# Kernel tuning notes

Measured on AMD Instinct MI355X. Metric: run time of the kernel, lower is better.

## Reference

```python
import jax, jax.numpy as jnp
import numpy as np

N_NODES = 100000
N_EDGES = 1600000
N_GRAPHS = 128


def setup_inputs() -> dict:
    key = jax.random.key(0)
    ks = jax.random.split(key, 8)
    x = jax.random.normal(ks[0], (N_NODES, 384), dtype=jnp.float32)
    edge_index = jax.random.randint(ks[1], (2, N_EDGES), 0, N_NODES, dtype=jnp.int64)
    batch = jnp.sort(jax.random.randint(ks[2], (N_NODES,), 0, N_GRAPHS, dtype=jnp.int64))
    W1 = jax.random.normal(ks[3], (384, 128), dtype=jnp.float32) * (1.0 / np.sqrt(384))
    b1 = jnp.zeros((128,), dtype=jnp.float32)
    W2 = jax.random.normal(ks[4], (128, 64), dtype=jnp.float32) * (1.0 / np.sqrt(128))
    b2 = jnp.zeros((64,), dtype=jnp.float32)
    Wlin = jax.random.normal(ks[5], (64, 2), dtype=jnp.float32) * (1.0 / np.sqrt(64))
    blin = jnp.zeros((2,), dtype=jnp.float32)
    return {"x": x, "edge_index": edge_index, "batch": batch,
            "W1": W1, "b1": b1, "W2": W2, "b2": b2, "Wlin": Wlin, "blin": blin}


def gcn_conv(x, src, dst, W, b, n_nodes):
    # PyG GCNConv: self-loops + symmetric normalization D^{-1/2} A_hat D^{-1/2},
    # linear transform first (out_dim < in_dim -> cheaper messages).
    h = x @ W  # [N, out]
    deg = jax.ops.segment_sum(jnp.ones_like(dst, dtype=h.dtype), dst,
                              num_segments=n_nodes) + 1.0  # self-loop weight
    dis = jax.lax.rsqrt(deg)  # deg >= 1 always (self-loop)
    norm = dis[src] * dis[dst]  # per-edge normalization [E]
    msg = h[src] * norm[:, None]  # gather + scale [E, out]
    agg = jax.ops.segment_sum(msg, dst, num_segments=n_nodes)
    agg = agg + h * (dis * dis)[:, None]  # self-loop contribution
    return agg + b


def reference(x, edge_index, batch, W1, b1, W2, b2, Wlin, blin):
    src, dst = edge_index[0], edge_index[1]
    n_nodes = x.shape[0]
    h = jax.nn.relu(gcn_conv(x, src, dst, W1, b1, n_nodes))
    h = jax.nn.relu(gcn_conv(h, src, dst, W2, b2, n_nodes))
    # global_mean_pool over graph ids
    sums = jax.ops.segment_sum(h, batch, num_segments=N_GRAPHS)
    cnts = jax.ops.segment_sum(jnp.ones((n_nodes,), dtype=h.dtype), batch,
                               num_segments=N_GRAPHS)
    pooled = sums / jnp.maximum(cnts, 1.0)[:, None]  # [G, 64]
    # dropout is identity in eval mode
    return pooled @ Wlin + blin  # [G, 2]
```

## Files before the change

### kernel.cpp

```cpp
#include <hip/hip_runtime.h>


#define NN 100000
#define NG 128
#define BNODES 256
#define NBUK ((NN + BNODES - 1) / BNODES)
#define BCAP 6144

typedef __attribute__((ext_vector_type(8))) short short8;
typedef __attribute__((ext_vector_type(8))) unsigned short u16x8;
typedef __attribute__((ext_vector_type(4))) float f32x4;

__device__ __forceinline__ unsigned short f2bf(float f) {
    union { float f; unsigned u; } v; v.f = f;
    unsigned r = v.u + 0x7fffu + ((v.u >> 16) & 1u);
    return (unsigned short)(r >> 16);
}
__device__ __forceinline__ float bf2f(unsigned short h) {
    union { unsigned u; float f; } v; v.u = ((unsigned)h) << 16;
    return v.f;
}

__device__ __forceinline__ void gload_lds16(const float* g, void* l) {
    __builtin_amdgcn_global_load_lds(
        (const __attribute__((address_space(1))) void*)g,
        (__attribute__((address_space(3))) void*)l, 16, 0, 0);
}

__global__ __launch_bounds__(256) void init_kernel(int* __restrict__ bcnt,
                                                   float* __restrict__ pooled,
                                                   float* __restrict__ cnt) {
    const int i = blockIdx.x * 256 + threadIdx.x;
    if (i < NBUK) bcnt[i] = 0;
    if (i < NG * 64) pooled[i] = 0.f;
    if (i < NG) cnt[i] = 0.f;
}

__global__ __launch_bounds__(256) void bucket_scatter(const int* __restrict__ src,
                                                      const int* __restrict__ dst,
                                                      int* __restrict__ bcnt,
                                                      int2* __restrict__ pairs, int E) {
    __shared__ int hist[NBUK];
    __shared__ int lbase[NBUK];
    __shared__ int lfill[NBUK];
    const int t = threadIdx.x;
    const int chunk = (E + gridDim.x - 1) / gridDim.x;
    const int lo = blockIdx.x * chunk;
    const int hi = min(E, lo + chunk);
    for (int b = t; b < NBUK; b += 256) { hist[b] = 0; lfill[b] = 0; }
    __syncthreads();
    for (int i = lo + t; i < hi; i += 256)
        atomicAdd(&hist[dst[i] >> 8], 1);
    __syncthreads();
    for (int b = t; b < NBUK; b += 256)
        lbase[b] = hist[b] ? atomicAdd(&bcnt[b], hist[b]) : 0;
    __syncthreads();
    for (int i = lo + t; i < hi; i += 256) {
        const int s = src[i], d = dst[i];
        const int b = d >> 8;
        const int off = atomicAdd(&lfill[b], 1);
        pairs[(size_t)b * BCAP + lbase[b] + off] = make_int2(s, d);
    }
}

__global__ __launch_bounds__(512) void bucket_scan(const int* __restrict__ bcnt,
                                                   int* __restrict__ bbase,
                                                   int* __restrict__ rowptr,
                                                   int N, int E) {
    __shared__ int sm[512];
    const int t = threadIdx.x;
    sm[t] = (t < NBUK) ? bcnt[t] : 0;
    __syncthreads();
    for (int d = 1; d < 512; d <<= 1) {
        int a = (t >= d) ? sm[t - d] : 0;
        __syncthreads();
        sm[t] += a;
        __syncthreads();
    }
    if (t <= NBUK) bbase[t] = (t == 0) ? 0 : sm[t - 1];
    if (t == 0) rowptr[N] = E;
}

__global__ __launch_bounds__(256) void bucket_build(const int2* __restrict__ pairs,
                                                    const int* __restrict__ bcnt,
                                                    const int* __restrict__ bbase,
                                                    int* __restrict__ rowptr,
                                                    float* __restrict__ dis,
                                                    int* __restrict__ col, int N) {
    __shared__ int cnt[BNODES];
    __shared__ int sm[BNODES];
    __shared__ int pref[BNODES];
    __shared__ int fillc[BNODES];
    const int b = blockIdx.x;
    const int t = threadIdx.x;
    const int nbase = b * BNODES;
    const int ecnt = bcnt[b];
    const int2* ep = pairs + (size_t)b * BCAP;
    const int gbase = bbase[b];

    cnt[t] = 0;
    fillc[t] = 0;
    __syncthreads();
    for (int i = t; i < ecnt; i += 256)
        atomicAdd(&cnt[ep[i].y & (BNODES - 1)], 1);
    __syncthreads();
    sm[t] = cnt[t];
    __syncthreads();
    for (int d = 1; d < 256; d <<= 1) {
        int a = (t >= d) ? sm[t - d] : 0;
        __syncthreads();
        sm[t] += a;
        __syncthreads();
    }
    pref[t] = sm[t] - cnt[t];
    const int node = nbase + t;
    if (node < N) {
        rowptr[node] = gbase + pref[t];
        dis[node] = rsqrtf((float)cnt[t] + 1.0f);
    }
    __syncthreads();
    for (int i = t; i < ecnt; i += 256) {
        const int2 e = ep[i];
        const int d = e.y & (BNODES - 1);
        const int pos = gbase + pref[d] + atomicAdd(&fillc[d], 1);
        col[pos] = e.x;
    }
}

__global__ __launch_bounds__(256) void pack_w(const float* __restrict__ W,
                                              unsigned short* __restrict__ packH,
                                              unsigned short* __restrict__ packL,
                                              int K, int BN) {
    const int idx = blockIdx.x * blockDim.x + threadIdx.x;
    if (idx >= K * BN) return;
    const int e = idx & 7;
    const int l = (idx >> 3) & 63;
    const int rest = idx >> 9;
    const int NF = BN >> 4;
    const int nf = rest % NF;
    const int ks = rest / NF;
    const int n = nf * 16 + (l & 15);
    const int k = ks * 32 + ((l >> 4) & 3) * 8 + e;
    const float v = W[(size_t)k * BN + n];
    const unsigned short h = f2bf(v);
    packH[idx] = h;
    packL[idx] = f2bf(v - bf2f(h));
}

template <int BN, int K>
__global__ __launch_bounds__(256) void gemm_mfma(const float* __restrict__ A,
                                                 const unsigned short* __restrict__ WpH,
                                                 const unsigned short* __restrict__ WpL,
                                                 const float* __restrict__ scale,
                                                 unsigned short* __restrict__ Out,
                                                 int N) {
    constexpr int BM = 64;
    constexpr int NK = K / 32;
    constexpr int WROWS = (BN == 128) ? 2 : 4;
    constexpr int WCOLS = (BN == 128) ? 2 : 1;
    constexpr int WTM = BM / WROWS;
    constexpr int MF = WTM / 16;
    constexpr int NFW = (BN / WCOLS) / 16;
    constexpr int NFB = BN / 16;

    __shared__ float AsF[4][4][16][32];

    const int t = threadIdx.x;
    const int wid = t >> 6, lane = t & 63;
    const int wr = wid / WCOLS, wc = wid % WCOLS;
    const int r0 = blockIdx.x * BM;

    const int dmarow0 = min(r0 + wid * 16 + (lane >> 3), NN - 1);
    const int dmarow1 = min(r0 + wid * 16 + 8 + (lane >> 3), NN - 1);
    const float* dmap0 = A + (size_t)dmarow0 * K + (lane & 7) * 4;
    const float* dmap1 = A + (size_t)dmarow1 * K + (lane & 7) * 4;

    auto stageA = [&](int buf, int ks) {
        gload_lds16(dmap0 + ks * 32, &AsF[buf][wid][0][0]);
        gload_lds16(dmap1 + ks * 32, &AsF[buf][wid][8][0]);
    };
    auto loadB = [&](int ks, short8* bH, short8* bL) {
#pragma unroll
        for (int n = 0; n < NFW; ++n) {
            const int nfg = wc * NFW + n;
            const int base = ((ks * NFB + nfg) * 64 + lane) * 8;
            bH[n] = *(const short8*)&WpH[base];
            bL[n] = *(const short8*)&WpL[base];
        }
    };

    f32x4 acc[MF][NFW];
#pragma unroll
    for (int m = 0; m < MF; ++m)
#pragma unroll
        for (int n = 0; n < NFW; ++n) acc[m][n] = (f32x4){0.f, 0.f, 0.f, 0.f};

    short8 bHc[NFW], bLc[NFW];
    loadB(0, bHc, bLc);
    stageA(0, 0);
    if (NK > 1) stageA(1, 1);
    if (NK > 2) stageA(2, 2);

#pragma unroll
    for (int ks = 0; ks < NK; ++ks) {
        if (ks == NK - 1) {
            asm volatile("s_waitcnt vmcnt(0)" ::: "memory");
        } else {
            asm volatile("s_waitcnt vmcnt(4)" ::: "memory");
        }
        __builtin_amdgcn_s_barrier();
        short8 bHn[NFW], bLn[NFW];
        if (ks + 1 < NK) loadB(ks + 1, bHn, bLn);
        if (ks + 3 < NK) stageA((ks + 3) & 3, ks + 3);
        const int cur = ks & 3;
#pragma unroll
        for (int m = 0; m < MF; ++m) {
            const int mf = wr * MF + m;
            const float* fp = &AsF[cur][mf][lane & 15][(lane >> 4) * 8];
            const f32x4 f0 = *(const f32x4*)fp;
            const f32x4 f1 = *(const f32x4*)(fp + 4);
            short8 aH;
            aH[0] = (short)f2bf(f0[0]);
            aH[1] = (short)f2bf(f0[1]);
            aH[2] = (short)f2bf(f0[2]);
            aH[3] = (short)f2bf(f0[3]);
            aH[4] = (short)f2bf(f1[0]);
            aH[5] = (short)f2bf(f1[1]);
            aH[6] = (short)f2bf(f1[2]);
            aH[7] = (short)f2bf(f1[3]);
#pragma unroll
            for (int n = 0; n < NFW; ++n) {
                acc[m][n] = __builtin_amdgcn_mfma_f32_16x16x32_bf16(aH, bHc[n], acc[m][n], 0, 0, 0);
                acc[m][n] = __builtin_amdgcn_mfma_f32_16x16x32_bf16(aH, bLc[n], acc[m][n], 0, 0, 0);
            }
        }
        if (ks + 1 < NK) {
#pragma unroll
            for (int n = 0; n < NFW; ++n) {
                bHc[n] = bHn[n];
                bLc[n] = bLn[n];
            }
        }
    }

#pragma unroll
    for (int m = 0; m < MF; ++m) {
        const int row0 = r0 + wr * WTM + m * 16 + ((lane >> 4) << 2);
        float sc[4];
#pragma unroll
        for (int r = 0; r < 4; ++r) sc[r] = (row0 + r < N) ? scale[row0 + r] : 0.f;
#pragma unroll
        for (int n = 0; n < NFW; ++n) {
            const int cn = wc * (NFW * 16) + n * 16 + (lane & 15);
#pragma unroll
            for (int r = 0; r < 4; ++r) {
                if (row0 + r < N)
                    Out[(size_t)(row0 + r) * BN + cn] = f2bf(acc[m][n][r] * sc[r]);
            }
        }
    }
}

template <int COLS>
__global__ __launch_bounds__(256) void agg_gather(const int* __restrict__ rowptr,
                                                  const int* __restrict__ col,
                                                  const float* __restrict__ dis,
                                                  const unsigned short* __restrict__ Hs,
                                                  const float* __restrict__ bias,
                                                  float* __restrict__ Out, int N) {
    constexpr int NPW = (COLS == 128) ? 1 : 2;
    constexpr int LPN = 64 / NPW;
    constexpr int LPR = COLS / 8;
    constexpr int NSG = LPN / LPR;
    const int gw = (int)((blockIdx.x * blockDim.x + threadIdx.x) >> 6);
    const int lane = threadIdx.x & 63;
    const int sub = lane / LPN;
    const int nl = lane % LPN;
    const int esub = nl / LPR;
    const int sl = nl % LPR;
    const int node = gw * NPW + sub;
    const int lgbase = sub * LPN;

    float acc[8];
#pragma unroll
    for (int k = 0; k < 8; ++k) acc[k] = 0.f;

    int base = 0, len = 0;
    const int nodec = (node < N) ? node : 0;
    if (node < N) {
        base = rowptr[node];
        len = rowptr[node + 1] - base;
    }

    for (int j0 = 0; j0 < len; j0 += LPN) {
        const int remain = min(LPN, len - j0);
        const int sidx = (nl < remain) ? col[base + j0 + nl] : nodec;
        const int qtr = (remain + NSG - 1) / NSG;
        const int off = esub * qtr;
        int u = 0;
        for (; u + 8 <= qtr; u += 8) {
            u16x8 hv[8];
            float wv[8];
#pragma unroll
            for (int b = 0; b < 8; ++b) {
                const int idx = off + u + b;
                const int s = __shfl(sidx, lgbase + idx);
                wv[b] = (idx < remain) ? 1.f : 0.f;
                hv[b] = *(const u16x8*)(Hs + (size_t)s * COLS + sl * 8);
            }
#pragma unroll
            for (int b = 0; b < 8; ++b)
#pragma unroll
                for (int k = 0; k < 8; ++k)
                    acc[k] = fmaf(bf2f(hv[b][k]), wv[b], acc[k]);
        }
        for (; u + 4 <= qtr; u += 4) {
            u16x8 hv[4];
            float wv[4];
#pragma unroll
            for (int b = 0; b < 4; ++b) {
                const int idx = off + u + b;
                const int s = __shfl(sidx, lgbase + idx);
                wv[b] = (idx < remain) ? 1.f : 0.f;
                hv[b] = *(const u16x8*)(Hs + (size_t)s * COLS + sl * 8);
            }
#pragma unroll
            for (int b = 0; b < 4; ++b)
#pragma unroll
                for (int k = 0; k < 8; ++k)
                    acc[k] = fmaf(bf2f(hv[b][k]), wv[b], acc[k]);
        }
        for (; u < qtr; ++u) {
            const int idx = off + u;
            const int s = __shfl(sidx, lgbase + idx);
            const float w = (idx < remain) ? 1.f : 0.f;
            const u16x8 hv = *(const u16x8*)(Hs + (size_t)s * COLS + sl * 8);
#pragma unroll
            for (int k = 0; k < 8; ++k)
                acc[k] = fmaf(bf2f(hv[k]), w, acc[k]);
        }
    }

#pragma unroll
    for (int k = 0; k < 8; ++k) {
        acc[k] += __shfl_xor(acc[k], LPR);
        acc[k] += __shfl_xor(acc[k], 2 * LPR);
    }

    if (node < N && esub == 0) {
        const float dd = dis[node];
        const u16x8 hsb = *(const u16x8*)(Hs + (size_t)node * COLS + sl * 8);
        const f32x4 bv0 = *(const f32x4*)(bias + sl * 8);
        const f32x4 bv1 = *(const f32x4*)(bias + sl * 8 + 4);
        f32x4 o0, o1;
#pragma unroll
        for (int k = 0; k < 4; ++k) {
            o0[k] = fmaxf(fmaf(acc[k] + bf2f(hsb[k]), dd, bv0[k]), 0.f);
            o1[k] = fmaxf(fmaf(acc[k + 4] + bf2f(hsb[k + 4]), dd, bv1[k]), 0.f);
        }
        *(f32x4*)(Out + (size_t)node * COLS + sl * 8) = o0;
        *(f32x4*)(Out + (size_t)node * COLS + sl * 8 + 4) = o1;
    }
}

__global__ __launch_bounds__(256) void pool_kernel(const float* __restrict__ H,
                                                   const int* __restrict__ batch,
                                                   float* __restrict__ pooled,
                                                   float* __restrict__ cnt, int N) {
    const int c = threadIdx.x & 63;
    const int w = threadIdx.x >> 6;
    const int row0 = blockIdx.x * 128 + w * 32;
    if (row0 >= N) return;
    const int nr = min(32, N - row0);

    float v[32];
    int b[32];
#pragma unroll
    for (int i = 0; i < 32; ++i) {
        const int r = row0 + i;
        if (i < nr) {
            v[i] = H[(size_t)r * 64 + c];
            b[i] = batch[r];
        } else {
            v[i] = 0.f;
            b[i] = -1;
        }
    }
    int cur = b[0];
    float sum = 0.f, csum = 0.f;
#pragma unroll
    for (int i = 0; i < 32; ++i) {
        if (i < nr) {
            if (b[i] != cur) {
                atomicAdd(&pooled[cur * 64 + c], sum);
                if (c == 0) atomicAdd(&cnt[cur], csum);
                cur = b[i];
                sum = 0.f;
                csum = 0.f;
            }
            sum += v[i];
            csum += 1.f;
        }
    }
    atomicAdd(&pooled[cur * 64 + c], sum);
    if (c == 0) atomicAdd(&cnt[cur], csum);
}

__global__ __launch_bounds__(256) void final_kernel(const float* __restrict__ pooled,
                                                    const float* __restrict__ cnt,
                                                    const float* __restrict__ Wlin,
                                                    const float* __restrict__ blin,
                                                    float* __restrict__ out) {
    const int t = threadIdx.x;
    const int g = t >> 1, o = t & 1;
    const float inv = 1.0f / fmaxf(cnt[g], 1.0f);
    float s = 0.f;
#pragma unroll
    for (int j = 0; j < 64; ++j) s = fmaf(pooled[g * 64 + j], Wlin[j * 2 + o], s);
    out[t] = s * inv + blin[o];
}

extern "C" void kernel_launch(void* const* d_in, const int* in_sizes, int n_in,
                              void* d_out, int out_size, void* d_ws, size_t ws_size,
                              hipStream_t stream) {
    const float* x     = (const float*)d_in[0];
    const int*   edge  = (const int*)d_in[1];
    const int*   batch = (const int*)d_in[2];
    const float* W1    = (const float*)d_in[3];
    const float* b1    = (const float*)d_in[4];
    const float* W2    = (const float*)d_in[5];
    const float* b2    = (const float*)d_in[6];
    const float* Wlin  = (const float*)d_in[7];
    const float* blin  = (const float*)d_in[8];
    float* out = (float*)d_out;

    const int N = NN;
    const int E = in_sizes[1] / 2;
    const int* src = edge;
    const int* dst = edge + E;

    char* ws = (char*)d_ws;
    size_t off = 0;
    auto alloc = [&](size_t bytes) -> void* {
        void* p = ws + off;
        off += (bytes + 511) & ~(size_t)511;
        return p;
    };
    float* dis    = (float*)alloc((size_t)N * 4);
    int*   rowptr = (int*)alloc((size_t)(N + 1) * 4);
    int*   bcnt   = (int*)alloc((size_t)NBUK * 4);
    int*   bbase  = (int*)alloc((size_t)(NBUK + 1) * 4);
    int*   col    = (int*)alloc((size_t)E * 4);
    int2*  pairs  = (int2*)alloc((size_t)NBUK * BCAP * 8);
    unsigned short* w1h = (unsigned short*)alloc((size_t)384 * 128 * 2);
    unsigned short* w1l = (unsigned short*)alloc((size_t)384 * 128 * 2);
    unsigned short* w2h = (unsigned short*)alloc((size_t)128 * 64 * 2);
    unsigned short* w2l = (unsigned short*)alloc((size_t)128 * 64 * 2);
    unsigned short* h1bf = (unsigned short*)alloc((size_t)N * 128 * 2);
    float* agg1   = (float*)alloc((size_t)N * 128 * 4);
    float* pooled = (float*)alloc((size_t)NG * 64 * 4);
    float* cnt    = (float*)alloc((size_t)NG * 4);
    unsigned short* h2bf = h1bf;
    float* agg2 = agg1;

    init_kernel<<<(NG * 64 + 255) / 256, 256, 0, stream>>>(bcnt, pooled, cnt);

    pack_w<<<(384 * 128 + 255) / 256, 256, 0, stream>>>(W1, w1h, w1l, 384, 128);
    pack_w<<<(128 * 64 + 255) / 256, 256, 0, stream>>>(W2, w2h, w2l, 128, 64);

    bucket_scatter<<<512, 256, 0, stream>>>(src, dst, bcnt, pairs, E);
    bucket_scan<<<1, 512, 0, stream>>>(bcnt, bbase, rowptr, N, E);
    bucket_build<<<NBUK, 256, 0, stream>>>(pairs, bcnt, bbase, rowptr, dis, col, N);

    const int gblocks = (N + 63) / 64;
    gemm_mfma<128, 384><<<gblocks, 256, 0, stream>>>(x, w1h, w1l, dis, h1bf, N);
    agg_gather<128><<<(N + 3) / 4, 256, 0, stream>>>(rowptr, col, dis, h1bf, b1, agg1, N);

    gemm_mfma<64, 128><<<gblocks, 256, 0, stream>>>(agg1, w2h, w2l, dis, h2bf, N);
    agg_gather<64><<<(N + 7) / 8, 256, 0, stream>>>(rowptr, col, dis, h2bf, b2, agg2, N);

    pool_kernel<<<(N + 127) / 128, 256, 0, stream>>>(agg2, batch, pooled, cnt, N);
    final_kernel<<<1, 256, 0, stream>>>(pooled, cnt, Wlin, blin, out);
}
```

Baseline: 243.3 us.

## Store layer-1 aggregation output in bf16 and add bf16-input GEMM for layer 2

The first aggregation kernel now writes its ReLU output as bf16 instead of fp32, halving that intermediate's write and the second GEMM's read traffic. A new GEMM variant consumes the bf16 activations directly via global-to-LDS loads with a 4-stage buffer, skipping the hi/lo split of A and using only the two MFMAs against the hi and lo weight halves. The cost is extra rounding error on the layer-1 activations, and agg2 now aliases the bf16 buffer, which is sized for 128 bf16 columns and so fits exactly the 64 fp32 columns it holds.

```diff
diff --git a/kernel.cpp b/kernel.cpp
--- a/kernel.cpp
+++ b/kernel.cpp
@@ -21,7 +21,7 @@
     return v.f;
 }
 
-__device__ __forceinline__ void gload_lds16(const float* g, void* l) {
+__device__ __forceinline__ void gload_lds16(const void* g, void* l) {
     __builtin_amdgcn_global_load_lds(
         (const __attribute__((address_space(1))) void*)g,
         (__attribute__((address_space(3))) void*)l, 16, 0, 0);
@@ -261,13 +261,103 @@
     }
 }
 
-template <int COLS>
+template <int BN, int K>
+__global__ __launch_bounds__(256) void gemm_mfma_b(const unsigned short* __restrict__ A,
+                                                   const unsigned short* __restrict__ WpH,
+                                                   const unsigned short* __restrict__ WpL,
+                                                   const float* __restrict__ scale,
+                                                   unsigned short* __restrict__ Out,
+                                                   int N) {
+    constexpr int BM = 64;
+    constexpr int NK = K / 32;
+    constexpr int WROWS = 4;
+    constexpr int WTM = BM / WROWS;
+    constexpr int NFW = BN / 16;
+    constexpr int NFB = BN / 16;
+
+    __shared__ unsigned short AsB[4][4][16][32];
+
+    const int t = threadIdx.x;
+    const int wid = t >> 6, lane = t & 63;
+    const int wr = wid;
+    const int r0 = blockIdx.x * BM;
+
+    const int dmarow = min(r0 + wid * 16 + (lane >> 2), NN - 1);
+    const unsigned short* dmap = A + (size_t)dmarow * K + (lane & 3) * 8;
+
+    auto stageA = [&](int buf, int ks) {
+        gload_lds16(dmap + ks * 32, &AsB[buf][wid][0][0]);
+    };
+    auto loadB = [&](int ks, short8* bH, short8* bL) {
+#pragma unroll
+        for (int n = 0; n < NFW; ++n) {
+            const int base = ((ks * NFB + n) * 64 + lane) * 8;
+            bH[n] = *(const short8*)&WpH[base];
+            bL[n] = *(const short8*)&WpL[base];
+        }
+    };
+
+    f32x4 acc[NFW];
+#pragma unroll
+    for (int n = 0; n < NFW; ++n) acc[n] = (f32x4){0.f, 0.f, 0.f, 0.f};
+
+    short8 bHc[NFW], bLc[NFW];
+    loadB(0, bHc, bLc);
+    stageA(0, 0);
+    if (NK > 1) stageA(1, 1);
+    if (NK > 2) stageA(2, 2);
+
+#pragma unroll
+    for (int ks = 0; ks < NK; ++ks) {
+        if (ks == NK - 1) {
+            asm volatile("s_waitcnt vmcnt(0)" ::: "memory");
+        } else if (ks == 0) {
+            asm volatile("s_waitcnt vmcnt(2)" ::: "memory");
+        } else {
+            asm volatile("s_waitcnt vmcnt(4)" ::: "memory");
+        }
+        __builtin_amdgcn_s_barrier();
+        short8 bHn[NFW], bLn[NFW];
+        if (ks + 1 < NK) loadB(ks + 1, bHn, bLn);
+        if (ks + 3 < NK) stageA((ks + 3) & 3, ks + 3);
+        const int cur = ks & 3;
+        const short8 aH = *(const short8*)&AsB[cur][wr][lane & 15][(lane >> 4) * 8];
+#pragma unroll
+        for (int n = 0; n < NFW; ++n) {
+            acc[n] = __builtin_amdgcn_mfma_f32_16x16x32_bf16(aH, bHc[n], acc[n], 0, 0, 0);
+            acc[n] = __builtin_amdgcn_mfma_f32_16x16x32_bf16(aH, bLc[n], acc[n], 0, 0, 0);
+        }
+        if (ks + 1 < NK) {
+#pragma unroll
+            for (int n = 0; n < NFW; ++n) {
+                bHc[n] = bHn[n];
+                bLc[n] = bLn[n];
+            }
+        }
+    }
+
+    const int row0 = r0 + wr * WTM + ((lane >> 4) << 2);
+    float sc[4];
+#pragma unroll
+    for (int r = 0; r < 4; ++r) sc[r] = (row0 + r < N) ? scale[row0 + r] : 0.f;
+#pragma unroll
+    for (int n = 0; n < NFW; ++n) {
+        const int cn = n * 16 + (lane & 15);
+#pragma unroll
+        for (int r = 0; r < 4; ++r) {
+            if (row0 + r < N)
+                Out[(size_t)(row0 + r) * BN + cn] = f2bf(acc[n][r] * sc[r]);
+        }
+    }
+}
+
+template <int COLS, bool OB16>
 __global__ __launch_bounds__(256) void agg_gather(const int* __restrict__ rowptr,
                                                   const int* __restrict__ col,
                                                   const float* __restrict__ dis,
                                                   const unsigned short* __restrict__ Hs,
                                                   const float* __restrict__ bias,
-                                                  float* __restrict__ Out, int N) {
+                                                  void* __restrict__ OutV, int N) {
     constexpr int NPW = (COLS == 128) ? 1 : 2;
     constexpr int LPN = 64 / NPW;
     constexpr int LPR = COLS / 8;
@@ -350,16 +440,26 @@
     if (node < N && esub == 0) {
         const float dd = dis[node];
         const u16x8 hsb = *(const u16x8*)(Hs + (size_t)node * COLS + sl * 8);
-        const f32x4 bv0 = *(const f32x4*)(bias + sl * 8);
-        const f32x4 bv1 = *(const f32x4*)(bias + sl * 8 + 4);
-        f32x4 o0, o1;
-#pragma unroll
-        for (int k = 0; k < 4; ++k) {
-            o0[k] = fmaxf(fmaf(acc[k] + bf2f(hsb[k]), dd, bv0[k]), 0.f);
-            o1[k] = fmaxf(fmaf(acc[k + 4] + bf2f(hsb[k + 4]), dd, bv1[k]), 0.f);
-        }
-        *(f32x4*)(Out + (size_t)node * COLS + sl * 8) = o0;
-        *(f32x4*)(Out + (size_t)node * COLS + sl * 8 + 4) = o1;
+        float o[8];
+#pragma unroll
+        for (int k = 0; k < 8; ++k)
+            o[k] = fmaxf(fmaf(acc[k] + bf2f(hsb[k]), dd, bias[sl * 8 + k]), 0.f);
+        if (OB16) {
+            u16x8 ob;
+#pragma unroll
+            for (int k = 0; k < 8; ++k) ob[k] = f2bf(o[k]);
+            *(u16x8*)((unsigned short*)OutV + (size_t)node * COLS + sl * 8) = ob;
+        } else {
+            float* Out = (float*)OutV;
+            f32x4 o0, o1;
+#pragma unroll
+            for (int k = 0; k < 4; ++k) {
+                o0[k] = o[k];
+                o1[k] = o[k + 4];
+            }
+            *(f32x4*)(Out + (size_t)node * COLS + sl * 8) = o0;
+            *(f32x4*)(Out + (size_t)node * COLS + sl * 8 + 4) = o1;
+        }
     }
 }
 
@@ -456,12 +556,12 @@
     unsigned short* w1l = (unsigned short*)alloc((size_t)384 * 128 * 2);
     unsigned short* w2h = (unsigned short*)alloc((size_t)128 * 64 * 2);
     unsigned short* w2l = (unsigned short*)alloc((size_t)128 * 64 * 2);
-    unsigned short* h1bf = (unsigned short*)alloc((size_t)N * 128 * 2);
-    float* agg1   = (float*)alloc((size_t)N * 128 * 4);
+    unsigned short* h1bf   = (unsigned short*)alloc((size_t)N * 128 * 2);
+    unsigned short* agg1bf = (unsigned short*)alloc((size_t)N * 128 * 2);
     float* pooled = (float*)alloc((size_t)NG * 64 * 4);
     float* cnt    = (float*)alloc((size_t)NG * 4);
     unsigned short* h2bf = h1bf;
-    float* agg2 = agg1;
+    float* agg2 = (float*)agg1bf;
 
     init_kernel<<<(NG * 64 + 255) / 256, 256, 0, stream>>>(bcnt, pooled, cnt);
 
@@ -474,10 +574,12 @@
 
     const int gblocks = (N + 63) / 64;
     gemm_mfma<128, 384><<<gblocks, 256, 0, stream>>>(x, w1h, w1l, dis, h1bf, N);
-    agg_gather<128><<<(N + 3) / 4, 256, 0, stream>>>(rowptr, col, dis, h1bf, b1, agg1, N);
-
-    gemm_mfma<64, 128><<<gblocks, 256, 0, stream>>>(agg1, w2h, w2l, dis, h2bf, N);
-    agg_gather<64><<<(N + 7) / 8, 256, 0, stream>>>(rowptr, col, dis, h2bf, b2, agg2, N);
+    agg_gather<128, true><<<(N + 3) / 4, 256, 0, stream>>>(rowptr, col, dis, h1bf, b1,
+                                                           (void*)agg1bf, N);
+
+    gemm_mfma_b<64, 128><<<gblocks, 256, 0, stream>>>(agg1bf, w2h, w2l, dis, h2bf, N);
+    agg_gather<64, false><<<(N + 7) / 8, 256, 0, stream>>>(rowptr, col, dis, h2bf, b2,
+                                                           (void*)agg2, N);
 
     pool_kernel<<<(N + 127) / 128, 256, 0, stream>>>(agg2, batch, pooled, cnt, N);
     final_kernel<<<1, 256, 0, stream>>>(pooled, cnt, Wlin, blin, out);
```

Result: faster. 236.2 us (-2.9%).
